# Performance work log

Hardware: AMD Instinct MI355X
Metric: run time of the kernel (lower is better)

Reference implementation:

```python
import jax, jax.numpy as jnp
import numpy as np

N_NODES = 5000
K_POOL = 30
BN_EPS = 1e-5


def setup_inputs() -> dict:
    key = jax.random.key(0)
    ks = jax.random.split(key, 16)
    B, N, Din, C, H, OUT, E = 32, N_NODES, 16, 64, 128, 2, 80000
    F_tot = Din + 3 * C  # concat of input + 3 conv layers = 208
    return {
        "x": jax.random.normal(ks[0], (B, N, Din), jnp.float32),
        "age": jax.random.uniform(ks[1], (B,), jnp.float32) * 100.0,
        "edge_attr": jax.random.uniform(ks[2], (E,), jnp.float32) + 0.1,
        "W0": jax.random.normal(ks[3], (Din, C), jnp.float32) * 0.1,
        "b0": jnp.zeros((C,), jnp.float32),
        "W1": jax.random.normal(ks[4], (C, C), jnp.float32) * 0.1,
        "b1": jnp.zeros((C,), jnp.float32),
        "W2": jax.random.normal(ks[5], (C, C), jnp.float32) * 0.1,
        "b2": jnp.zeros((C,), jnp.float32),
        "g0": jnp.ones((C,), jnp.float32),
        "be0": jnp.zeros((C,), jnp.float32),
        "g1": jnp.ones((C,), jnp.float32),
        "be1": jnp.zeros((C,), jnp.float32),
        "mW0": jax.random.normal(ks[6], (K_POOL * F_tot + 1, H), jnp.float32) * 0.02,
        "mb0": jnp.zeros((H,), jnp.float32),
        "mW1": jax.random.normal(ks[7], (H, OUT), jnp.float32) * 0.1,
        "mb1": jnp.zeros((OUT,), jnp.float32),
        "edge_row": jax.random.randint(ks[8], (E,), 0, N, jnp.int32),
        "edge_col": jax.random.randint(ks[9], (E,), 0, N, jnp.int32),
    }


def _spmm(xw, rows, cols, nv):
    # xw: (B, N, C); out[b, r] = sum_{edges (r,c)} nv * xw[b, c]
    def one(xb):
        return jax.ops.segment_sum(xb[cols] * nv[:, None], rows, num_segments=N_NODES)
    return jax.vmap(one)(xw)


def reference(x, age, edge_attr, W0, b0, W1, b1, W2, b2, g0, be0, g1, be1,
              mW0, mb0, mW1, mb1, edge_row, edge_col):
    N = N_NODES
    # GCN normalization on A + I (gcn_norm with edge weights, self-loop value 1)
    loop = jnp.arange(N, dtype=edge_row.dtype)
    rows = jnp.concatenate([edge_row, loop])
    cols = jnp.concatenate([edge_col, loop])
    vals = jnp.concatenate([edge_attr, jnp.ones((N,), edge_attr.dtype)])
    deg = jax.ops.segment_sum(vals, rows, num_segments=N)
    dinv = jnp.where(deg > 0, jax.lax.rsqrt(jnp.maximum(deg, 1e-12)), 0.0)
    nv = dinv[rows] * vals * dinv[cols]

    feats = [x]
    h = x
    convs = [(W0, b0), (W1, b1), (W2, b2)]
    bns = [(g0, be0), (g1, be1)]
    for i, (W, b) in enumerate(convs):
        h = _spmm(h @ W, rows, cols, nv) + b  # GCNConv
        if i < len(convs) - 1:
            g, be = bns[i]
            mu = jnp.mean(h, axis=(0, 1))   # BatchNorm1d over flattened (B*N, C)
            var = jnp.var(h, axis=(0, 1))
            h = (h - mu) * jax.lax.rsqrt(var + BN_EPS) * g + be
        h = jax.nn.relu(h)  # dropout p=0.0 -> identity
        feats.append(h)

    z = jnp.concatenate(feats, axis=-1)  # (B, N, 208)
    # global_sort_pool: sort nodes by last feature channel, descending, take top-k
    order = jnp.argsort(-z[:, :, -1], axis=1)[:, :K_POOL]  # (B, k)
    zk = jnp.take_along_axis(z, order[:, :, None], axis=1)  # (B, k, 208)
    flat = zk.reshape(z.shape[0], -1)
    flat = jnp.concatenate([flat, age[:, None]], axis=1)  # append age scalar

    hm = jax.nn.relu(flat @ mW0 + mb0)  # MLP head
    out = hm @ mW1 + mb1
    return jax.nn.log_softmax(out, axis=-1)
```

## Files before the change

kernel.cpp:

```cpp
#include <hip/hip_runtime.h>
#include <math.h>

#define NN    5000
#define NE    80000
#define NB    32
#define DIN   16
#define CH    64
#define KPOOL 30
#define FTOT  208
#define FLATW 6241
#define NH    128
#define NG    8
#define GB    4
#define NPB   16
#define NCHUNK 313
#define NPAD  5008
#define NEPAD (NE + 4 * NN)
#define NSLOT 32



__global__ void k_init(float* deg, int* counts, float* stats, float* hm, int* perm) {
    int i = blockIdx.x * 256 + threadIdx.x;
    if (i < NN) { deg[i] = 1.0f; counts[i] = 0; }
    if (i < 2 * NSLOT * 128) stats[i] = 0.0f;
    if (i < 4096) hm[i] = 0.0f;
    if (i >= NN && i < NPAD) perm[i] = NN;
}

#define NEB 313
__global__ void k_edges(const float* __restrict__ attr, const int* __restrict__ erow,
                        float* deg, int* counts) {
    int e = blockIdx.x * 256 + threadIdx.x;
    if (e < NE) {
        int r = erow[e];
        atomicAdd(&deg[r], attr[e]);
        atomicAdd(&counts[r], 1);
    }
}

__global__ __launch_bounds__(1024) void k_phase1(
        const int* __restrict__ counts, const float* __restrict__ deg,
        int* rowptr, int* cursor, float* dinv, int* perm,
        const float* __restrict__ x, float* __restrict__ xt) {
    __shared__ int wsum[16], woff[16];
    __shared__ int carry_sh;
    __shared__ int hist[256];
    int t = threadIdx.x;
    if (blockIdx.x >= 2) {
        int idx = (blockIdx.x - 2) * 1024 + t;
        if (idx >= NB * NN) return;
        int b = idx / NN, n = idx % NN;
        int g = b >> 2, bi = b & 3;
        const float4* src = (const float4*)(x + (size_t)idx * DIN);
        float4* dst = (float4*)(xt + (((size_t)g * NN + n) * GB + bi) * DIN);
        dst[0] = src[0]; dst[1] = src[1]; dst[2] = src[2]; dst[3] = src[3];
        return;
    }
    if (blockIdx.x == 0) {
        int lane = t & 63, wid = t >> 6;
        if (t == 0) carry_sh = 0;
        __syncthreads();
        for (int base = 0; base < NN; base += 1024) {
            int carry = carry_sh;
            int i = base + t;
            int v = 0;
            if (i < NN) {
                v = (counts[i] + 3) & ~3;
                dinv[i] = 1.0f / sqrtf(deg[i]);
            }
            int s = v;
#pragma unroll
            for (int off = 1; off < 64; off <<= 1) {
                int o = __shfl_up(s, off);
                if (lane >= off) s += o;
            }
            if (lane == 63) wsum[wid] = s;
            __syncthreads();
            if (t < 16) {
                int w = wsum[t];
#pragma unroll
                for (int off = 1; off < 16; off <<= 1) {
                    int o = __shfl_up(w, off);
                    if (t >= off) w += o;
                }
                woff[t] = w;
            }
            __syncthreads();
            int inc = s + (wid > 0 ? woff[wid - 1] : 0) + carry;
            if (i < NN) {
                rowptr[i + 1] = inc;
                cursor[i] = inc - v;
            }
            if (t == 1023) carry_sh = carry + woff[15];
            __syncthreads();
        }
        if (t == 0) rowptr[0] = 0;
    } else {
        if (t < 256) hist[t] = 0;
        __syncthreads();
        for (int i = t; i < NN; i += 1024) {
            int b = 255 - min(((counts[i] + 3) & ~3) >> 2, 255);
            atomicAdd(&hist[b], 1);
        }
        __syncthreads();
        int mycnt = (t < 256) ? hist[t] : 0;
        for (int off = 1; off < 256; off <<= 1) {
            int v = (t < 256 && t >= off) ? hist[t - off] : 0;
            __syncthreads();
            if (t < 256) hist[t] += v;
            __syncthreads();
        }
        if (t < 256) hist[t] -= mycnt;
        __syncthreads();
        for (int i = t; i < NN; i += 1024) {
            int b = 255 - min(((counts[i] + 3) & ~3) >> 2, 255);
            int pos = atomicAdd(&hist[b], 1);
            perm[pos] = i;
        }
    }
}

__global__ __launch_bounds__(1024) void k_build(
        const int* __restrict__ erow, const int* __restrict__ ecol,
        const float* __restrict__ attr, const float* __restrict__ dinv,
        const int* __restrict__ counts, const int* __restrict__ rowptr,
        int* cursor, int* csr_col, float* csr_nv) {
    int t = blockIdx.x * 1024 + threadIdx.x;
    if (t < NE) {
        int r = erow[t], c = ecol[t];
        int pos = atomicAdd(&cursor[r], 1);
        csr_col[pos] = c;
        csr_nv[pos] = dinv[r] * attr[t] * dinv[c];
    } else if (t - NE < NN) {
        int i = t - NE;
        int cnt = counts[i];
        int pcnt = (cnt + 3) & ~3;
        int base = rowptr[i + 1] - pcnt;
        for (int p = base + cnt; p < base + pcnt; ++p) { csr_col[p] = i; csr_nv[p] = 0.0f; }
    }
}

template<int ACT>
__device__ __forceinline__ float4 actv(float4 v, float4 s, float4 t) {
    if (ACT) {
        v.x = fmaxf(fmaf(v.x, s.x, t.x), 0.f);
        v.y = fmaxf(fmaf(v.y, s.y, t.y), 0.f);
        v.z = fmaxf(fmaf(v.z, s.z, t.z), 0.f);
        v.w = fmaxf(fmaf(v.w, s.w, t.w), 0.f);
    }
    return v;
}
__device__ __forceinline__ void fma4(float4& a, float w, float4 v) {
    a.x = fmaf(w, v.x, a.x); a.y = fmaf(w, v.y, a.y);
    a.z = fmaf(w, v.z, a.z); a.w = fmaf(w, v.w, a.w);
}

template<int CIN, int ACT, int STATS>
__global__ __launch_bounds__(256) void k_layer(
        const float* __restrict__ in, const float* __restrict__ bnstats,
        const float* __restrict__ gamma, const float* __restrict__ beta,
        const float* __restrict__ W, const float* __restrict__ bias,
        const int* __restrict__ rowptr, const int* __restrict__ csr_col,
        const float* __restrict__ csr_nv, const float* __restrict__ dinv,
        const int* __restrict__ perm,
        float* __restrict__ out, float* __restrict__ stats) {
    constexpr int ALS = (CIN == 64) ? 68 : 20;
    __shared__ float As[4 * 16 * ALS];
    __shared__ float stl[ACT ? 128 : 4];
    int tid = threadIdx.x;
    int wid = tid >> 6, lane = tid & 63;
    int g = blockIdx.x & 7;
    int nb = (blockIdx.x >> 3) * NPB;
    int base = nb + wid * 4;
    float* Aw = As + wid * 16 * ALS;
    const int4 pid = *(const int4*)(perm + base);

    if (ACT) {
        if (tid < 64) {
            float su = 0.f, qu = 0.f;
#pragma unroll
            for (int s = 0; s < NSLOT; ++s) {
                su += bnstats[s * 128 + tid];
                qu += bnstats[s * 128 + 64 + tid];
            }
            const float inv = 1.0f / (float)(NB * NN);
            float mu = su * inv;
            float var = qu * inv - mu * mu;
            float sc = gamma[tid] / sqrtf(var + 1e-5f);
            stl[tid] = sc;
            stl[64 + tid] = fmaf(-mu, sc, beta[tid]);
        }
        __syncthreads();
    }

    if (CIN == 64) {
        const float4* __restrict__ in4 = (const float4*)in + (size_t)g * NN * 64;
        int c4 = lane & 15, bi = lane >> 4;
        float4 sv = {1.f,1.f,1.f,1.f}, tv = {0.f,0.f,0.f,0.f};
        if (ACT) { sv = ((const float4*)stl)[c4]; tv = ((const float4*)(stl + 64))[c4]; }
#pragma unroll
        for (int pr = 0; pr < 2; ++pr) {
            int id0 = (pr == 0) ? pid.x : pid.z;
            int id1 = (pr == 0) ? pid.y : pid.w;
            bool vn0 = id0 < NN, vn1 = id1 < NN;
            int rc0 = vn0 ? id0 : 0, rc1 = vn1 ? id1 : 0;
            float dd0 = dinv[rc0]; dd0 *= dd0;
            float dd1 = dinv[rc1]; dd1 *= dd1;
            float4 a0 = {0.f,0.f,0.f,0.f}, a1 = {0.f,0.f,0.f,0.f};
            {
                float4 v0 = actv<ACT>(in4[(size_t)rc0 * 64 + lane], sv, tv);
                float4 v1 = actv<ACT>(in4[(size_t)rc1 * 64 + lane], sv, tv);
                if (vn0) { a0.x = dd0 * v0.x; a0.y = dd0 * v0.y; a0.z = dd0 * v0.z; a0.w = dd0 * v0.w; }
                if (vn1) { a1.x = dd1 * v1.x; a1.y = dd1 * v1.y; a1.z = dd1 * v1.z; a1.w = dd1 * v1.w; }
            }
            int p0a = rowptr[rc0], na = vn0 ? (rowptr[rc0 + 1] - p0a) >> 2 : 0;
            int p0b = rowptr[rc1], nbv = vn1 ? (rowptr[rc1 + 1] - p0b) >> 2 : 0;
            int mx = max(na, nbv);
            for (int bb = 0; bb < mx; ++bb) {
                int ea = min(p0a + 4 * bb, NEPAD - 4);
                int eb = min(p0b + 4 * bb, NEPAD - 4);
                bool va = bb < na, vb = bb < nbv;
                int4   ca = *(const int4*)(csr_col + ea);
                float4 wa = *(const float4*)(csr_nv + ea);
                int4   cb = *(const int4*)(csr_col + eb);
                float4 wb = *(const float4*)(csr_nv + eb);
                if (!va) { wa.x = 0.f; wa.y = 0.f; wa.z = 0.f; wa.w = 0.f;
                           ca.x = 0; ca.y = 0; ca.z = 0; ca.w = 0; }
                if (!vb) { wb.x = 0.f; wb.y = 0.f; wb.z = 0.f; wb.w = 0.f;
                           cb.x = 0; cb.y = 0; cb.z = 0; cb.w = 0; }
                float4 u0 = in4[(size_t)ca.x * 64 + lane];
                float4 u1 = in4[(size_t)ca.y * 64 + lane];
                float4 u2 = in4[(size_t)ca.z * 64 + lane];
                float4 u3 = in4[(size_t)ca.w * 64 + lane];
                float4 t0 = in4[(size_t)cb.x * 64 + lane];
                float4 t1 = in4[(size_t)cb.y * 64 + lane];
                float4 t2 = in4[(size_t)cb.z * 64 + lane];
                float4 t3 = in4[(size_t)cb.w * 64 + lane];
                fma4(a0, wa.x, actv<ACT>(u0, sv, tv));
                fma4(a0, wa.y, actv<ACT>(u1, sv, tv));
                fma4(a0, wa.z, actv<ACT>(u2, sv, tv));
                fma4(a0, wa.w, actv<ACT>(u3, sv, tv));
                fma4(a1, wb.x, actv<ACT>(t0, sv, tv));
                fma4(a1, wb.y, actv<ACT>(t1, sv, tv));
                fma4(a1, wb.z, actv<ACT>(t2, sv, tv));
                fma4(a1, wb.w, actv<ACT>(t3, sv, tv));
            }
            *(float4*)(Aw + ((pr * 2 + 0) * 4 + bi) * ALS + c4 * 4) = a0;
            *(float4*)(Aw + ((pr * 2 + 1) * 4 + bi) * ALS + c4 * 4) = a1;
        }
    } else {
        const float* __restrict__ inr = in + (size_t)g * NN * 64;
        int ids[4] = {pid.x, pid.y, pid.z, pid.w};
#pragma unroll
        for (int i = 0; i < 4; ++i) {
            int r = ids[i];
            float a = 0.f;
            if (r < NN) {
                float d = dinv[r];
                a = d * d * inr[(size_t)r * 64 + lane];
                int p0 = rowptr[r], p1 = rowptr[r + 1];
                for (int e = p0; e < p1; e += 4) {
                    int4   cc = *(const int4*)(csr_col + e);
                    float4 ww = *(const float4*)(csr_nv + e);
                    float v0 = inr[(size_t)cc.x * 64 + lane];
                    float v1 = inr[(size_t)cc.y * 64 + lane];
                    float v2 = inr[(size_t)cc.z * 64 + lane];
                    float v3 = inr[(size_t)cc.w * 64 + lane];
                    a = fmaf(ww.x, v0, a);
                    a = fmaf(ww.y, v1, a);
                    a = fmaf(ww.z, v2, a);
                    a = fmaf(ww.w, v3, a);
                }
            }
            Aw[(i * 4 + (lane >> 4)) * ALS + (lane & 15)] = a;
        }
    }

    int colq = lane & 15, rowq = lane >> 4;
    int node = (rowq == 0) ? pid.x : (rowq == 1) ? pid.y : (rowq == 2) ? pid.z : pid.w;

    const float4* __restrict__ W4 = (const float4*)W;
    float4 bb = ((const float4*)bias)[colq];
    float4 o[4];
#pragma unroll
    for (int i = 0; i < 4; ++i) o[i] = bb;
#pragma unroll 8
    for (int k = 0; k < CIN; ++k) {
        float4 w4 = W4[k * 16 + colq];
#pragma unroll
        for (int i = 0; i < 4; ++i) {
            float a = Aw[(rowq * 4 + i) * ALS + k];
            fma4(o[i], a, w4);
        }
    }
    if (node < NN) {
        float4* __restrict__ op = (float4*)(out + ((size_t)g * NN + node) * 256);
#pragma unroll
        for (int i = 0; i < 4; ++i) op[i * 16 + colq] = o[i];
    }

    if (STATS) {
        float4 s4 = {0,0,0,0}, q4 = {0,0,0,0};
        if (node < NN) {
#pragma unroll
            for (int i = 0; i < 4; ++i) {
                s4.x += o[i].x; s4.y += o[i].y; s4.z += o[i].z; s4.w += o[i].w;
                q4.x = fmaf(o[i].x, o[i].x, q4.x); q4.y = fmaf(o[i].y, o[i].y, q4.y);
                q4.z = fmaf(o[i].z, o[i].z, q4.z); q4.w = fmaf(o[i].w, o[i].w, q4.w);
            }
        }
        s4.x += __shfl_xor(s4.x, 16); s4.y += __shfl_xor(s4.y, 16);
        s4.z += __shfl_xor(s4.z, 16); s4.w += __shfl_xor(s4.w, 16);
        q4.x += __shfl_xor(q4.x, 16); q4.y += __shfl_xor(q4.y, 16);
        q4.z += __shfl_xor(q4.z, 16); q4.w += __shfl_xor(q4.w, 16);
        s4.x += __shfl_xor(s4.x, 32); s4.y += __shfl_xor(s4.y, 32);
        s4.z += __shfl_xor(s4.z, 32); s4.w += __shfl_xor(s4.w, 32);
        q4.x += __shfl_xor(q4.x, 32); q4.y += __shfl_xor(q4.y, 32);
        q4.z += __shfl_xor(q4.z, 32); q4.w += __shfl_xor(q4.w, 32);
        __syncthreads();
        if (lane < 16) {
            float* S = As + wid * 128;
            *(float4*)(S + lane * 8) = s4;
            *(float4*)(S + lane * 8 + 4) = q4;
        }
        __syncthreads();
        if (tid < 64) {
            int cq = tid >> 2, comp = tid & 3;
            float s = 0.f, q = 0.f;
#pragma unroll
            for (int w = 0; w < 4; ++w) {
                s += As[w * 128 + cq * 8 + comp];
                q += As[w * 128 + cq * 8 + 4 + comp];
            }
            float* sl = stats + (blockIdx.x & (NSLOT - 1)) * 128;
            atomicAdd(&sl[tid], s);
            atomicAdd(&sl[64 + tid], q);
        }
    }
}

#define ZBLK 2048
__global__ __launch_bounds__(256) void k_z(
        const float* __restrict__ h2, const float* __restrict__ bnstats,
        const float* __restrict__ gamma, const float* __restrict__ beta,
        const float* __restrict__ W2, float* __restrict__ z) {
    __shared__ float stl[128];
    __shared__ float w63[64];
    int tid = threadIdx.x;
    if (tid < 64) {
        float su = 0.f, qu = 0.f;
#pragma unroll
        for (int s = 0; s < NSLOT; ++s) {
            su += bnstats[s * 128 + tid];
            qu += bnstats[s * 128 + 64 + tid];
        }
        const float inv = 1.0f / (float)(NB * NN);
        float mu = su * inv;
        float var = qu * inv - mu * mu;
        float sc = gamma[tid] / sqrtf(var + 1e-5f);
        stl[tid] = sc;
        stl[64 + tid] = fmaf(-mu, sc, beta[tid]);
        w63[tid] = W2[tid * 64 + 63];
    }
    __syncthreads();
    int lane = tid & 63, wid = tid >> 6;
    int c4 = lane & 15;
    float4 sv = ((const float4*)stl)[c4];
    float4 tv = ((const float4*)(stl + 64))[c4];
    float4 w4 = ((const float4*)w63)[c4];
    const int total = NB * NN;
    for (int base = blockIdx.x * 16; base < total; base += ZBLK * 16) {
        int row = base + wid * 4 + (lane >> 4);
        float s = 0.f;
        if (row < total) {
            float4 v = ((const float4*)h2)[(size_t)row * 16 + c4];
            v.x = fmaxf(fmaf(v.x, sv.x, tv.x), 0.f);
            v.y = fmaxf(fmaf(v.y, sv.y, tv.y), 0.f);
            v.z = fmaxf(fmaf(v.z, sv.z, tv.z), 0.f);
            v.w = fmaxf(fmaf(v.w, sv.w, tv.w), 0.f);
            s = v.x * w4.x + v.y * w4.y + v.z * w4.z + v.w * w4.w;
        }
        s += __shfl_xor(s, 1);
        s += __shfl_xor(s, 2);
        s += __shfl_xor(s, 4);
        s += __shfl_xor(s, 8);
        if ((lane & 15) == 0 && row < total) z[row] = s;
    }
}

__global__ __launch_bounds__(256) void k_score(
        const float* __restrict__ z, const float* __restrict__ b2,
        const int* __restrict__ rowptr, const int* __restrict__ csr_col,
        const float* __restrict__ csr_nv, const float* __restrict__ dinv,
        float* __restrict__ sc) {
    int tid = threadIdx.x;
    int wid = tid >> 6, lane = tid & 63;
    int g = blockIdx.x & 7;
    int nd = (blockIdx.x >> 3) * 4 + wid;
    if (nd >= NN) return;
    const float4* __restrict__ z4 = (const float4*)z + (size_t)g * NN;
    int p0 = rowptr[nd], p1 = rowptr[nd + 1];
    float4 a = {0.f, 0.f, 0.f, 0.f};
    for (int e = p0 + lane; e < p1; e += 64) {
        int col = csr_col[e];
        float nv = csr_nv[e];
        float4 zv = z4[col];
        fma4(a, nv, zv);
    }
#pragma unroll
    for (int off = 1; off < 64; off <<= 1) {
        a.x += __shfl_xor(a.x, off);
        a.y += __shfl_xor(a.y, off);
        a.z += __shfl_xor(a.z, off);
        a.w += __shfl_xor(a.w, off);
    }
    if (lane == 0) {
        float d = dinv[nd]; d *= d;
        float4 zs = z4[nd];
        float bb = b2[63];
        float4 o;
        o.x = fmaxf(fmaf(d, zs.x, a.x) + bb, 0.f);
        o.y = fmaxf(fmaf(d, zs.y, a.y) + bb, 0.f);
        o.z = fmaxf(fmaf(d, zs.z, a.z) + bb, 0.f);
        o.w = fmaxf(fmaf(d, zs.w, a.w) + bb, 0.f);
        ((float4*)sc)[(size_t)g * NN + nd] = o;
    }
}

__global__ __launch_bounds__(1024) void k_toppool(const float* __restrict__ sc, int* order,
        const float* __restrict__ stats,
        const float* __restrict__ g0, const float* __restrict__ be0,
        const float* __restrict__ g1, const float* __restrict__ be1,
        float* __restrict__ st) {
    __shared__ unsigned long long wbest[16];
    __shared__ unsigned long long winner;
    int tid = threadIdx.x;
    if (blockIdx.x == NB) {
        if (tid < 128) {
            int c = tid & 63, layer = tid >> 6;
            const float* sb = stats + layer * NSLOT * 128;
            float su = 0.f, qu = 0.f;
#pragma unroll
            for (int s = 0; s < NSLOT; ++s) {
                su += sb[s * 128 + c];
                qu += sb[s * 128 + 64 + c];
            }
            const float inv = 1.0f / (float)(NB * NN);
            float mu = su * inv;
            float var = qu * inv - mu * mu;
            float g = layer ? g1[c] : g0[c];
            float be = layer ? be1[c] : be0[c];
            float scv = g / sqrtf(var + 1e-5f);
            st[layer * 128 + c] = scv;
            st[layer * 128 + 64 + c] = fmaf(-mu, scv, be);
        }
        return;
    }
    int b = blockIdx.x;
    int g = b >> 2, bi = b & 3;
    int lane = tid & 63, wid = tid >> 6;
    unsigned long long key[5];
#pragma unroll
    for (int j = 0; j < 5; ++j) {
        int n = tid + j * 1024;
        unsigned long long k = 0;
        if (n < NN) {
            float v = sc[((size_t)g * NN + n) * GB + bi];
            k = ((unsigned long long)__float_as_uint(v) << 32) | (unsigned int)(NN - n);
        }
        key[j] = k;
    }
    for (int k = 0; k < KPOOL; ++k) {
        unsigned long long best = key[0];
#pragma unroll
        for (int j = 1; j < 5; ++j) best = (key[j] > best) ? key[j] : best;
#pragma unroll
        for (int off = 1; off < 64; off <<= 1) {
            unsigned long long o = __shfl_xor(best, off);
            best = (o > best) ? o : best;
        }
        if (lane == 0) wbest[wid] = best;
        __syncthreads();
        if (tid == 0) {
            unsigned long long w = wbest[0];
#pragma unroll
            for (int i = 1; i < 16; ++i) w = (wbest[i] > w) ? wbest[i] : w;
            winner = w;
            order[b * KPOOL + k] = NN - (int)(w & 0xFFFFFFFFu);
        }
        __syncthreads();
        int n = NN - (int)(winner & 0xFFFFFFFFu);
        if ((n & 1023) == tid) key[n >> 10] = 0;
    }
}

__global__ void k_gather(const float* __restrict__ xt, const float* __restrict__ h1,
                         const float* __restrict__ h2,
                         const float* __restrict__ W2, const float* __restrict__ b2,
                         const float* __restrict__ st, const float* __restrict__ age,
                         const int* __restrict__ rowptr, const int* __restrict__ csr_col,
                         const float* __restrict__ csr_nv, const float* __restrict__ dinv,
                         const int* __restrict__ order, float* __restrict__ flat) {
    __shared__ float aggP[4][64];
    __shared__ float aggRow[64];
    int bk = blockIdx.x;
    int b = bk / KPOOL, k = bk % KPOOL;
    int n = order[bk];
    int g = b >> 2, bi = b & 3;
    size_t node = (size_t)g * NN + n;
    int tid = threadIdx.x;
    {
        int ep = tid >> 6, c = tid & 63;
        float sc1 = st[128 + c], sh1 = st[192 + c];
        float a = 0.f;
        if (ep == 0) {
            float d = dinv[n];
            float v = h2[(node * GB + bi) * CH + c];
            a = d * d * fmaxf(fmaf(v, sc1, sh1), 0.f);
        }
        int p0 = rowptr[n], p1 = rowptr[n + 1];
        for (int e = p0 + ep; e < p1; e += 4) {
            int col = csr_col[e];
            float nv = csr_nv[e];
            float v = h2[(((size_t)g * NN + col) * GB + bi) * CH + c];
            a += nv * fmaxf(fmaf(v, sc1, sh1), 0.f);
        }
        aggP[ep][c] = a;
    }
    __syncthreads();
    if (tid < 64) aggRow[tid] = aggP[0][tid] + aggP[1][tid] + aggP[2][tid] + aggP[3][tid];
    __syncthreads();
    int f = tid;
    float val = 0.f;
    if (f < DIN) {
        val = xt[(node * GB + bi) * DIN + f];
    } else if (f < DIN + CH) {
        int c = f - DIN;
        val = fmaxf(fmaf(h1[(node * GB + bi) * CH + c], st[c], st[64 + c]), 0.f);
    } else if (f < DIN + 2 * CH) {
        int c = f - DIN - CH;
        val = fmaxf(fmaf(h2[(node * GB + bi) * CH + c], st[128 + c], st[192 + c]), 0.f);
    } else if (f < FTOT) {
        int c = f - DIN - 2 * CH;
        float s = b2[c];
#pragma unroll 8
        for (int kk = 0; kk < 64; ++kk)
            s = fmaf(aggRow[kk], W2[kk * 64 + c], s);
        val = fmaxf(s, 0.f);
    }
    if (f < FTOT) flat[(size_t)b * FLATW + k * FTOT + f] = val;
    if (bk == 0 && f >= FTOT && f < FTOT + NB)
        flat[(size_t)(f - FTOT) * FLATW + (FLATW - 1)] = age[f - FTOT];
}

__global__ void k_head1(const float* __restrict__ flat, const float* __restrict__ mW0,
                        float* hm) {
    int tid = threadIdx.x;
    int j4 = (tid & 31) * 4;
    int b0 = (tid >> 5) * 4;
    int kbase = blockIdx.x * 64;
    float acc[4][4];
#pragma unroll
    for (int i = 0; i < 4; i++)
#pragma unroll
        for (int jj = 0; jj < 4; jj++) acc[i][jj] = 0.f;
    int kend = FLATW - kbase; if (kend > 64) kend = 64;
    for (int kk = 0; kk < kend; ++kk) {
        int k = kbase + kk;
        float4 w = *(const float4*)(mW0 + (size_t)k * NH + j4);
#pragma unroll
        for (int i = 0; i < 4; i++) {
            float fv = flat[(size_t)(b0 + i) * FLATW + k];
            acc[i][0] = fmaf(fv, w.x, acc[i][0]);
            acc[i][1] = fmaf(fv, w.y, acc[i][1]);
            acc[i][2] = fmaf(fv, w.z, acc[i][2]);
            acc[i][3] = fmaf(fv, w.w, acc[i][3]);
        }
    }
#pragma unroll
    for (int i = 0; i < 4; i++)
#pragma unroll
        for (int jj = 0; jj < 4; jj++)
            atomicAdd(&hm[(size_t)(b0 + i) * NH + j4 + jj], acc[i][jj]);
}

__global__ void k_head2(const float* __restrict__ hm, const float* __restrict__ mb0,
                        const float* __restrict__ mW1, const float* __restrict__ mb1,
                        float* __restrict__ out) {
    __shared__ float part[256];
    __shared__ float vals[64];
    int tid = threadIdx.x;
    int q = tid & 3, o = (tid >> 2) & 1, b = tid >> 3;
    float acc = 0.f;
    for (int j = q * 32; j < q * 32 + 32; ++j) {
        float hv = fmaxf(hm[b * NH + j] + mb0[j], 0.f);
        acc = fmaf(hv, mW1[j * 2 + o], acc);
    }
    part[tid] = acc;
    __syncthreads();
    if (tid < 64) {
        int b2 = tid >> 1, o2 = tid & 1;
        int base = (b2 << 3) + (o2 << 2);
        vals[tid] = part[base] + part[base + 1] + part[base + 2] + part[base + 3] + mb1[o2];
    }
    __syncthreads();
    if (tid < 64) {
        int b2 = tid >> 1;
        float v0 = vals[b2 * 2], v1 = vals[b2 * 2 + 1];
        float m = fmaxf(v0, v1);
        float lse = m + logf(expf(v0 - m) + expf(v1 - m));
        out[tid] = vals[tid] - lse;
    }
}

extern "C" void kernel_launch(void* const* d_in, const int* in_sizes, int n_in,
                              void* d_out, int out_size, void* d_ws, size_t ws_size,
                              hipStream_t stream) {
    const float* x    = (const float*)d_in[0];
    const float* age  = (const float*)d_in[1];
    const float* attr = (const float*)d_in[2];
    const float* W0   = (const float*)d_in[3];
    const float* b0   = (const float*)d_in[4];
    const float* W1   = (const float*)d_in[5];
    const float* b1   = (const float*)d_in[6];
    const float* W2   = (const float*)d_in[7];
    const float* b2   = (const float*)d_in[8];
    const float* g0   = (const float*)d_in[9];
    const float* be0  = (const float*)d_in[10];
    const float* g1   = (const float*)d_in[11];
    const float* be1  = (const float*)d_in[12];
    const float* mW0  = (const float*)d_in[13];
    const float* mb0  = (const float*)d_in[14];
    const float* mW1  = (const float*)d_in[15];
    const float* mb1  = (const float*)d_in[16];
    const int* erow   = (const int*)d_in[17];
    const int* ecol   = (const int*)d_in[18];
    float* out = (float*)d_out;

    float* ws     = (float*)d_ws;
    float* deg    = ws;
    float* dinv   = deg + 5008;
    int*   counts = (int*)(dinv + 5008);
    int*   rowptr = counts + 5008;
    int*   cursor = rowptr + 5008;
    int*   perm   = cursor + 5008;
    int*   csr_col= perm + 5008;
    float* csr_nv = (float*)(csr_col + NEPAD);
    float* stats  = csr_nv + NEPAD;
    float* st     = stats + 2 * NSLOT * 128;
    float* sc     = st + 256;
    int*   order  = (int*)(sc + NB * NN);
    float* flat   = (float*)(order + 960);
    float* hm     = flat + (size_t)NB * FLATW;
    float* xt     = hm + 4096;
    float* h1     = xt + (size_t)NB * NN * DIN;
    float* h2     = h1 + (size_t)NB * NN * CH;
    float* z      = h2 + (size_t)NB * NN * CH;

    k_init<<<32, 256, 0, stream>>>(deg, counts, stats, hm, perm);
    k_edges<<<NEB, 256, 0, stream>>>(attr, erow, deg, counts);
    k_phase1<<<2 + (NB * NN + 1023) / 1024, 1024, 0, stream>>>(counts, deg, rowptr, cursor, dinv, perm, x, xt);
    k_build<<<(NE + NN + 1023) / 1024, 1024, 0, stream>>>(erow, ecol, attr, dinv, counts, rowptr, cursor, csr_col, csr_nv);

    const int NBLK = NCHUNK * NG;
    k_layer<16, 0, 1><<<NBLK, 256, 0, stream>>>(xt, nullptr, nullptr, nullptr, W0, b0, rowptr, csr_col, csr_nv, dinv, perm, h1, stats);
    k_layer<64, 1, 1><<<NBLK, 256, 0, stream>>>(h1, stats, g0, be0, W1, b1, rowptr, csr_col, csr_nv, dinv, perm, h2, stats + NSLOT * 128);
    k_z<<<ZBLK, 256, 0, stream>>>(h2, stats + NSLOT * 128, g1, be1, W2, z);
    k_score<<<(NN / 4) * NG, 256, 0, stream>>>(z, b2, rowptr, csr_col, csr_nv, dinv, sc);

    k_toppool<<<NB + 1, 1024, 0, stream>>>(sc, order, stats, g0, be0, g1, be1, st);
    k_gather<<<NB * KPOOL, 256, 0, stream>>>(xt, h1, h2, W2, b2, st, age, rowptr, csr_col, csr_nv, dinv, order, flat);
    k_head1<<<(FLATW + 63) / 64, 256, 0, stream>>>(flat, mW0, hm);
    k_head2<<<1, 256, 0, stream>>>(hm, mb0, mW1, mb1, out);
}
```

Measured before the change: 316.5 us.

## Regroup input into 8-batch groups and specialize first GCN layer with float2 gathers

Changes the transposed input layout from 4-batch to 8-batch groups so each 64-lane wavefront gathers a full neighbor row (8 batches x 16 channels) as float2 per lane. It adds a dedicated first-layer kernel that processes 8 batches per block with half as many blocks. The old template splits into separate 16- and 64-channel kernels. The aim is better-utilized, wider gathers and fewer redundant CSR index loads in layer 0. In exchange it uses more registers for 8 output accumulators, and the gather kernel's read of the input must follow the new layout.

```diff
diff --git a/kernel.cpp b/kernel.cpp
--- a/kernel.cpp
+++ b/kernel.cpp
@@ -51,9 +51,9 @@
         int idx = (blockIdx.x - 2) * 1024 + t;
         if (idx >= NB * NN) return;
         int b = idx / NN, n = idx % NN;
-        int g = b >> 2, bi = b & 3;
+        int g4 = b >> 3, bi8 = b & 7;
         const float4* src = (const float4*)(x + (size_t)idx * DIN);
-        float4* dst = (float4*)(xt + (((size_t)g * NN + n) * GB + bi) * DIN);
+        float4* dst = (float4*)(xt + (((size_t)g4 * NN + n) * 8 + bi8) * DIN);
         dst[0] = src[0]; dst[1] = src[1]; dst[2] = src[2]; dst[3] = src[3];
         return;
     }
@@ -141,23 +141,154 @@
     }
 }
 
-template<int ACT>
 __device__ __forceinline__ float4 actv(float4 v, float4 s, float4 t) {
-    if (ACT) {
-        v.x = fmaxf(fmaf(v.x, s.x, t.x), 0.f);
-        v.y = fmaxf(fmaf(v.y, s.y, t.y), 0.f);
-        v.z = fmaxf(fmaf(v.z, s.z, t.z), 0.f);
-        v.w = fmaxf(fmaf(v.w, s.w, t.w), 0.f);
-    }
+    v.x = fmaxf(fmaf(v.x, s.x, t.x), 0.f);
+    v.y = fmaxf(fmaf(v.y, s.y, t.y), 0.f);
+    v.z = fmaxf(fmaf(v.z, s.z, t.z), 0.f);
+    v.w = fmaxf(fmaf(v.w, s.w, t.w), 0.f);
     return v;
 }
 __device__ __forceinline__ void fma4(float4& a, float w, float4 v) {
     a.x = fmaf(w, v.x, a.x); a.y = fmaf(w, v.y, a.y);
     a.z = fmaf(w, v.z, a.z); a.w = fmaf(w, v.w, a.w);
 }
-
-template<int CIN, int ACT, int STATS>
-__global__ __launch_bounds__(256) void k_layer(
+__device__ __forceinline__ void fma2(float2& a, float w, float2 v) {
+    a.x = fmaf(w, v.x, a.x); a.y = fmaf(w, v.y, a.y);
+}
+
+__global__ __launch_bounds__(256) void k_l16(
+        const float* __restrict__ in,
+        const float* __restrict__ W, const float* __restrict__ bias,
+        const int* __restrict__ rowptr, const int* __restrict__ csr_col,
+        const float* __restrict__ csr_nv, const float* __restrict__ dinv,
+        const int* __restrict__ perm,
+        float* __restrict__ out, float* __restrict__ stats) {
+    const int ALS = 18;
+    __shared__ float As[4 * 32 * ALS];
+    int tid = threadIdx.x;
+    int wid = tid >> 6, lane = tid & 63;
+    int g4 = blockIdx.x & 3;
+    int base = (blockIdx.x >> 2) * NPB + wid * 4;
+    float* Aw = As + wid * 32 * ALS;
+    const int4 pid = *(const int4*)(perm + base);
+
+    const float2* __restrict__ in2 = (const float2*)in + (size_t)g4 * NN * 64;
+    int bi8 = lane >> 3, chp = lane & 7;
+
+#pragma unroll
+    for (int pr = 0; pr < 2; ++pr) {
+        int id0 = (pr == 0) ? pid.x : pid.z;
+        int id1 = (pr == 0) ? pid.y : pid.w;
+        bool vn0 = id0 < NN, vn1 = id1 < NN;
+        int rc0 = vn0 ? id0 : 0, rc1 = vn1 ? id1 : 0;
+        float dd0 = dinv[rc0]; dd0 *= dd0;
+        float dd1 = dinv[rc1]; dd1 *= dd1;
+        float2 a0 = {0.f, 0.f}, a1 = {0.f, 0.f};
+        {
+            float2 v0 = in2[(size_t)rc0 * 64 + lane];
+            float2 v1 = in2[(size_t)rc1 * 64 + lane];
+            if (vn0) { a0.x = dd0 * v0.x; a0.y = dd0 * v0.y; }
+            if (vn1) { a1.x = dd1 * v1.x; a1.y = dd1 * v1.y; }
+        }
+        int p0a = rowptr[rc0], na = vn0 ? (rowptr[rc0 + 1] - p0a) >> 2 : 0;
+        int p0b = rowptr[rc1], nbv = vn1 ? (rowptr[rc1 + 1] - p0b) >> 2 : 0;
+        int mx = max(na, nbv);
+        for (int bb = 0; bb < mx; ++bb) {
+            int ea = min(p0a + 4 * bb, NEPAD - 4);
+            int eb = min(p0b + 4 * bb, NEPAD - 4);
+            bool va = bb < na, vb = bb < nbv;
+            int4   ca = *(const int4*)(csr_col + ea);
+            float4 wa = *(const float4*)(csr_nv + ea);
+            int4   cb = *(const int4*)(csr_col + eb);
+            float4 wb = *(const float4*)(csr_nv + eb);
+            if (!va) { wa.x = 0.f; wa.y = 0.f; wa.z = 0.f; wa.w = 0.f;
+                       ca.x = 0; ca.y = 0; ca.z = 0; ca.w = 0; }
+            if (!vb) { wb.x = 0.f; wb.y = 0.f; wb.z = 0.f; wb.w = 0.f;
+                       cb.x = 0; cb.y = 0; cb.z = 0; cb.w = 0; }
+            float2 u0 = in2[(size_t)ca.x * 64 + lane];
+            float2 u1 = in2[(size_t)ca.y * 64 + lane];
+            float2 u2 = in2[(size_t)ca.z * 64 + lane];
+            float2 u3 = in2[(size_t)ca.w * 64 + lane];
+            float2 t0 = in2[(size_t)cb.x * 64 + lane];
+            float2 t1 = in2[(size_t)cb.y * 64 + lane];
+            float2 t2 = in2[(size_t)cb.z * 64 + lane];
+            float2 t3 = in2[(size_t)cb.w * 64 + lane];
+            fma2(a0, wa.x, u0);
+            fma2(a0, wa.y, u1);
+            fma2(a0, wa.z, u2);
+            fma2(a0, wa.w, u3);
+            fma2(a1, wb.x, t0);
+            fma2(a1, wb.y, t1);
+            fma2(a1, wb.z, t2);
+            fma2(a1, wb.w, t3);
+        }
+        *(float2*)(Aw + ((2 * pr + 0) * 8 + bi8) * ALS + chp * 2) = a0;
+        *(float2*)(Aw + ((2 * pr + 1) * 8 + bi8) * ALS + chp * 2) = a1;
+    }
+
+    int colq = lane & 15, rowq = lane >> 4;
+    int node = (rowq == 0) ? pid.x : (rowq == 1) ? pid.y : (rowq == 2) ? pid.z : pid.w;
+
+    const float4* __restrict__ W4 = (const float4*)W;
+    float4 bb4 = ((const float4*)bias)[colq];
+    float4 o[8];
+#pragma unroll
+    for (int i = 0; i < 8; ++i) o[i] = bb4;
+#pragma unroll
+    for (int k = 0; k < 16; ++k) {
+        float4 w4 = W4[k * 16 + colq];
+#pragma unroll
+        for (int i = 0; i < 8; ++i)
+            fma4(o[i], Aw[(rowq * 8 + i) * ALS + k], w4);
+    }
+    if (node < NN) {
+#pragma unroll
+        for (int i = 0; i < 8; ++i) {
+            int g8 = g4 * 2 + (i >> 2);
+            float4* op = (float4*)(out + (((size_t)g8 * NN + node) * 4 + (i & 3)) * 64);
+            op[colq] = o[i];
+        }
+    }
+
+    float4 s4 = {0,0,0,0}, q4 = {0,0,0,0};
+    if (node < NN) {
+#pragma unroll
+        for (int i = 0; i < 8; ++i) {
+            s4.x += o[i].x; s4.y += o[i].y; s4.z += o[i].z; s4.w += o[i].w;
+            q4.x = fmaf(o[i].x, o[i].x, q4.x); q4.y = fmaf(o[i].y, o[i].y, q4.y);
+            q4.z = fmaf(o[i].z, o[i].z, q4.z); q4.w = fmaf(o[i].w, o[i].w, q4.w);
+        }
+    }
+    s4.x += __shfl_xor(s4.x, 16); s4.y += __shfl_xor(s4.y, 16);
+    s4.z += __shfl_xor(s4.z, 16); s4.w += __shfl_xor(s4.w, 16);
+    q4.x += __shfl_xor(q4.x, 16); q4.y += __shfl_xor(q4.y, 16);
+    q4.z += __shfl_xor(q4.z, 16); q4.w += __shfl_xor(q4.w, 16);
+    s4.x += __shfl_xor(s4.x, 32); s4.y += __shfl_xor(s4.y, 32);
+    s4.z += __shfl_xor(s4.z, 32); s4.w += __shfl_xor(s4.w, 32);
+    q4.x += __shfl_xor(q4.x, 32); q4.y += __shfl_xor(q4.y, 32);
+    q4.z += __shfl_xor(q4.z, 32); q4.w += __shfl_xor(q4.w, 32);
+    __syncthreads();
+    if (lane < 16) {
+        float* S = As + wid * 128;
+        *(float4*)(S + lane * 8) = s4;
+        *(float4*)(S + lane * 8 + 4) = q4;
+    }
+    __syncthreads();
+    if (tid < 64) {
+        int cq = tid >> 2, comp = tid & 3;
+        float s = 0.f, q = 0.f;
+#pragma unroll
+        for (int w = 0; w < 4; ++w) {
+            s += As[w * 128 + cq * 8 + comp];
+            q += As[w * 128 + cq * 8 + 4 + comp];
+        }
+        float* sl = stats + (blockIdx.x & (NSLOT - 1)) * 128;
+        atomicAdd(&sl[tid], s);
+        atomicAdd(&sl[64 + tid], q);
+    }
+}
+
+__global__ __launch_bounds__(256) void k_l64(
         const float* __restrict__ in, const float* __restrict__ bnstats,
         const float* __restrict__ gamma, const float* __restrict__ beta,
         const float* __restrict__ W, const float* __restrict__ bias,
@@ -165,116 +296,85 @@
         const float* __restrict__ csr_nv, const float* __restrict__ dinv,
         const int* __restrict__ perm,
         float* __restrict__ out, float* __restrict__ stats) {
-    constexpr int ALS = (CIN == 64) ? 68 : 20;
+    const int ALS = 68;
     __shared__ float As[4 * 16 * ALS];
-    __shared__ float stl[ACT ? 128 : 4];
+    __shared__ float stl[128];
     int tid = threadIdx.x;
     int wid = tid >> 6, lane = tid & 63;
     int g = blockIdx.x & 7;
-    int nb = (blockIdx.x >> 3) * NPB;
-    int base = nb + wid * 4;
+    int base = (blockIdx.x >> 3) * NPB + wid * 4;
     float* Aw = As + wid * 16 * ALS;
     const int4 pid = *(const int4*)(perm + base);
 
-    if (ACT) {
-        if (tid < 64) {
-            float su = 0.f, qu = 0.f;
-#pragma unroll
-            for (int s = 0; s < NSLOT; ++s) {
-                su += bnstats[s * 128 + tid];
-                qu += bnstats[s * 128 + 64 + tid];
-            }
-            const float inv = 1.0f / (float)(NB * NN);
-            float mu = su * inv;
-            float var = qu * inv - mu * mu;
-            float sc = gamma[tid] / sqrtf(var + 1e-5f);
-            stl[tid] = sc;
-            stl[64 + tid] = fmaf(-mu, sc, beta[tid]);
-        }
-        __syncthreads();
-    }
-
-    if (CIN == 64) {
-        const float4* __restrict__ in4 = (const float4*)in + (size_t)g * NN * 64;
-        int c4 = lane & 15, bi = lane >> 4;
-        float4 sv = {1.f,1.f,1.f,1.f}, tv = {0.f,0.f,0.f,0.f};
-        if (ACT) { sv = ((const float4*)stl)[c4]; tv = ((const float4*)(stl + 64))[c4]; }
-#pragma unroll
-        for (int pr = 0; pr < 2; ++pr) {
-            int id0 = (pr == 0) ? pid.x : pid.z;
-            int id1 = (pr == 0) ? pid.y : pid.w;
-            bool vn0 = id0 < NN, vn1 = id1 < NN;
-            int rc0 = vn0 ? id0 : 0, rc1 = vn1 ? id1 : 0;
-            float dd0 = dinv[rc0]; dd0 *= dd0;
-            float dd1 = dinv[rc1]; dd1 *= dd1;
-            float4 a0 = {0.f,0.f,0.f,0.f}, a1 = {0.f,0.f,0.f,0.f};
-            {
-                float4 v0 = actv<ACT>(in4[(size_t)rc0 * 64 + lane], sv, tv);
-                float4 v1 = actv<ACT>(in4[(size_t)rc1 * 64 + lane], sv, tv);
-                if (vn0) { a0.x = dd0 * v0.x; a0.y = dd0 * v0.y; a0.z = dd0 * v0.z; a0.w = dd0 * v0.w; }
-                if (vn1) { a1.x = dd1 * v1.x; a1.y = dd1 * v1.y; a1.z = dd1 * v1.z; a1.w = dd1 * v1.w; }
-            }
-            int p0a = rowptr[rc0], na = vn0 ? (rowptr[rc0 + 1] - p0a) >> 2 : 0;
-            int p0b = rowptr[rc1], nbv = vn1 ? (rowptr[rc1 + 1] - p0b) >> 2 : 0;
-            int mx = max(na, nbv);
-            for (int bb = 0; bb < mx; ++bb) {
-                int ea = min(p0a + 4 * bb, NEPAD - 4);
-                int eb = min(p0b + 4 * bb, NEPAD - 4);
-                bool va = bb < na, vb = bb < nbv;
-                int4   ca = *(const int4*)(csr_col + ea);
-                float4 wa = *(const float4*)(csr_nv + ea);
-                int4   cb = *(const int4*)(csr_col + eb);
-                float4 wb = *(const float4*)(csr_nv + eb);
-                if (!va) { wa.x = 0.f; wa.y = 0.f; wa.z = 0.f; wa.w = 0.f;
-                           ca.x = 0; ca.y = 0; ca.z = 0; ca.w = 0; }
-                if (!vb) { wb.x = 0.f; wb.y = 0.f; wb.z = 0.f; wb.w = 0.f;
-                           cb.x = 0; cb.y = 0; cb.z = 0; cb.w = 0; }
-                float4 u0 = in4[(size_t)ca.x * 64 + lane];
-                float4 u1 = in4[(size_t)ca.y * 64 + lane];
-                float4 u2 = in4[(size_t)ca.z * 64 + lane];
-                float4 u3 = in4[(size_t)ca.w * 64 + lane];
-                float4 t0 = in4[(size_t)cb.x * 64 + lane];
-                float4 t1 = in4[(size_t)cb.y * 64 + lane];
-                float4 t2 = in4[(size_t)cb.z * 64 + lane];
-                float4 t3 = in4[(size_t)cb.w * 64 + lane];
-                fma4(a0, wa.x, actv<ACT>(u0, sv, tv));
-                fma4(a0, wa.y, actv<ACT>(u1, sv, tv));
-                fma4(a0, wa.z, actv<ACT>(u2, sv, tv));
-                fma4(a0, wa.w, actv<ACT>(u3, sv, tv));
-                fma4(a1, wb.x, actv<ACT>(t0, sv, tv));
-                fma4(a1, wb.y, actv<ACT>(t1, sv, tv));
-                fma4(a1, wb.z, actv<ACT>(t2, sv, tv));
-                fma4(a1, wb.w, actv<ACT>(t3, sv, tv));
-            }
-            *(float4*)(Aw + ((pr * 2 + 0) * 4 + bi) * ALS + c4 * 4) = a0;
-            *(float4*)(Aw + ((pr * 2 + 1) * 4 + bi) * ALS + c4 * 4) = a1;
-        }
-    } else {
-        const float* __restrict__ inr = in + (size_t)g * NN * 64;
-        int ids[4] = {pid.x, pid.y, pid.z, pid.w};
-#pragma unroll
-        for (int i = 0; i < 4; ++i) {
-            int r = ids[i];
-            float a = 0.f;
-            if (r < NN) {
-                float d = dinv[r];
-                a = d * d * inr[(size_t)r * 64 + lane];
-                int p0 = rowptr[r], p1 = rowptr[r + 1];
-                for (int e = p0; e < p1; e += 4) {
-                    int4   cc = *(const int4*)(csr_col + e);
-                    float4 ww = *(const float4*)(csr_nv + e);
-                    float v0 = inr[(size_t)cc.x * 64 + lane];
-                    float v1 = inr[(size_t)cc.y * 64 + lane];
-                    float v2 = inr[(size_t)cc.z * 64 + lane];
-                    float v3 = inr[(size_t)cc.w * 64 + lane];
-                    a = fmaf(ww.x, v0, a);
-                    a = fmaf(ww.y, v1, a);
-                    a = fmaf(ww.z, v2, a);
-                    a = fmaf(ww.w, v3, a);
-                }
-            }
-            Aw[(i * 4 + (lane >> 4)) * ALS + (lane & 15)] = a;
-        }
+    if (tid < 64) {
+        float su = 0.f, qu = 0.f;
+#pragma unroll
+        for (int s = 0; s < NSLOT; ++s) {
+            su += bnstats[s * 128 + tid];
+            qu += bnstats[s * 128 + 64 + tid];
+        }
+        const float inv = 1.0f / (float)(NB * NN);
+        float mu = su * inv;
+        float var = qu * inv - mu * mu;
+        float sc = gamma[tid] / sqrtf(var + 1e-5f);
+        stl[tid] = sc;
+        stl[64 + tid] = fmaf(-mu, sc, beta[tid]);
+    }
+    __syncthreads();
+
+    const float4* __restrict__ in4 = (const float4*)in + (size_t)g * NN * 64;
+    int c4 = lane & 15, bi = lane >> 4;
+    float4 sv = ((const float4*)stl)[c4];
+    float4 tv = ((const float4*)(stl + 64))[c4];
+#pragma unroll
+    for (int pr = 0; pr < 2; ++pr) {
+        int id0 = (pr == 0) ? pid.x : pid.z;
+        int id1 = (pr == 0) ? pid.y : pid.w;
+        bool vn0 = id0 < NN, vn1 = id1 < NN;
+        int rc0 = vn0 ? id0 : 0, rc1 = vn1 ? id1 : 0;
+        float dd0 = dinv[rc0]; dd0 *= dd0;
+        float dd1 = dinv[rc1]; dd1 *= dd1;
+        float4 a0 = {0.f,0.f,0.f,0.f}, a1 = {0.f,0.f,0.f,0.f};
+        {
+            float4 v0 = actv(in4[(size_t)rc0 * 64 + lane], sv, tv);
+            float4 v1 = actv(in4[(size_t)rc1 * 64 + lane], sv, tv);
+            if (vn0) { a0.x = dd0 * v0.x; a0.y = dd0 * v0.y; a0.z = dd0 * v0.z; a0.w = dd0 * v0.w; }
+            if (vn1) { a1.x = dd1 * v1.x; a1.y = dd1 * v1.y; a1.z = dd1 * v1.z; a1.w = dd1 * v1.w; }
+        }
+        int p0a = rowptr[rc0], na = vn0 ? (rowptr[rc0 + 1] - p0a) >> 2 : 0;
+        int p0b = rowptr[rc1], nbv = vn1 ? (rowptr[rc1 + 1] - p0b) >> 2 : 0;
+        int mx = max(na, nbv);
+        for (int bb = 0; bb < mx; ++bb) {
+            int ea = min(p0a + 4 * bb, NEPAD - 4);
+            int eb = min(p0b + 4 * bb, NEPAD - 4);
+            bool va = bb < na, vb = bb < nbv;
+            int4   ca = *(const int4*)(csr_col + ea);
+            float4 wa = *(const float4*)(csr_nv + ea);
+            int4   cb = *(const int4*)(csr_col + eb);
+            float4 wb = *(const float4*)(csr_nv + eb);
+            if (!va) { wa.x = 0.f; wa.y = 0.f; wa.z = 0.f; wa.w = 0.f;
+                       ca.x = 0; ca.y = 0; ca.z = 0; ca.w = 0; }
+            if (!vb) { wb.x = 0.f; wb.y = 0.f; wb.z = 0.f; wb.w = 0.f;
+                       cb.x = 0; cb.y = 0; cb.z = 0; cb.w = 0; }
+            float4 u0 = in4[(size_t)ca.x * 64 + lane];
+            float4 u1 = in4[(size_t)ca.y * 64 + lane];
+            float4 u2 = in4[(size_t)ca.z * 64 + lane];
+            float4 u3 = in4[(size_t)ca.w * 64 + lane];
+            float4 t0 = in4[(size_t)cb.x * 64 + lane];
+            float4 t1 = in4[(size_t)cb.y * 64 + lane];
+            float4 t2 = in4[(size_t)cb.z * 64 + lane];
+            float4 t3 = in4[(size_t)cb.w * 64 + lane];
+            fma4(a0, wa.x, actv(u0, sv, tv));
+            fma4(a0, wa.y, actv(u1, sv, tv));
+            fma4(a0, wa.z, actv(u2, sv, tv));
+            fma4(a0, wa.w, actv(u3, sv, tv));
+            fma4(a1, wb.x, actv(t0, sv, tv));
+            fma4(a1, wb.y, actv(t1, sv, tv));
+            fma4(a1, wb.z, actv(t2, sv, tv));
+            fma4(a1, wb.w, actv(t3, sv, tv));
+        }
+        *(float4*)(Aw + ((pr * 2 + 0) * 4 + bi) * ALS + c4 * 4) = a0;
+        *(float4*)(Aw + ((pr * 2 + 1) * 4 + bi) * ALS + c4 * 4) = a1;
     }
 
     int colq = lane & 15, rowq = lane >> 4;
@@ -286,7 +386,7 @@
 #pragma unroll
     for (int i = 0; i < 4; ++i) o[i] = bb;
 #pragma unroll 8
-    for (int k = 0; k < CIN; ++k) {
+    for (int k = 0; k < 64; ++k) {
         float4 w4 = W4[k * 16 + colq];
 #pragma unroll
         for (int i = 0; i < 4; ++i) {
@@ -300,43 +400,41 @@
         for (int i = 0; i < 4; ++i) op[i * 16 + colq] = o[i];
     }
 
-    if (STATS) {
-        float4 s4 = {0,0,0,0}, q4 = {0,0,0,0};
-        if (node < NN) {
-#pragma unroll
-            for (int i = 0; i < 4; ++i) {
-                s4.x += o[i].x; s4.y += o[i].y; s4.z += o[i].z; s4.w += o[i].w;
-                q4.x = fmaf(o[i].x, o[i].x, q4.x); q4.y = fmaf(o[i].y, o[i].y, q4.y);
-                q4.z = fmaf(o[i].z, o[i].z, q4.z); q4.w = fmaf(o[i].w, o[i].w, q4.w);
-            }
-        }
-        s4.x += __shfl_xor(s4.x, 16); s4.y += __shfl_xor(s4.y, 16);
-        s4.z += __shfl_xor(s4.z, 16); s4.w += __shfl_xor(s4.w, 16);
-        q4.x += __shfl_xor(q4.x, 16); q4.y += __shfl_xor(q4.y, 16);
-        q4.z += __shfl_xor(q4.z, 16); q4.w += __shfl_xor(q4.w, 16);
-        s4.x += __shfl_xor(s4.x, 32); s4.y += __shfl_xor(s4.y, 32);
-        s4.z += __shfl_xor(s4.z, 32); s4.w += __shfl_xor(s4.w, 32);
-        q4.x += __shfl_xor(q4.x, 32); q4.y += __shfl_xor(q4.y, 32);
-        q4.z += __shfl_xor(q4.z, 32); q4.w += __shfl_xor(q4.w, 32);
-        __syncthreads();
-        if (lane < 16) {
-            float* S = As + wid * 128;
-            *(float4*)(S + lane * 8) = s4;
-            *(float4*)(S + lane * 8 + 4) = q4;
-        }
-        __syncthreads();
-        if (tid < 64) {
-            int cq = tid >> 2, comp = tid & 3;
-            float s = 0.f, q = 0.f;
-#pragma unroll
-            for (int w = 0; w < 4; ++w) {
-                s += As[w * 128 + cq * 8 + comp];
-                q += As[w * 128 + cq * 8 + 4 + comp];
-            }
-            float* sl = stats + (blockIdx.x & (NSLOT - 1)) * 128;
-            atomicAdd(&sl[tid], s);
-            atomicAdd(&sl[64 + tid], q);
-        }
+    float4 s4 = {0,0,0,0}, q4 = {0,0,0,0};
+    if (node < NN) {
+#pragma unroll
+        for (int i = 0; i < 4; ++i) {
+            s4.x += o[i].x; s4.y += o[i].y; s4.z += o[i].z; s4.w += o[i].w;
+            q4.x = fmaf(o[i].x, o[i].x, q4.x); q4.y = fmaf(o[i].y, o[i].y, q4.y);
+            q4.z = fmaf(o[i].z, o[i].z, q4.z); q4.w = fmaf(o[i].w, o[i].w, q4.w);
+        }
+    }
+    s4.x += __shfl_xor(s4.x, 16); s4.y += __shfl_xor(s4.y, 16);
+    s4.z += __shfl_xor(s4.z, 16); s4.w += __shfl_xor(s4.w, 16);
+    q4.x += __shfl_xor(q4.x, 16); q4.y += __shfl_xor(q4.y, 16);
+    q4.z += __shfl_xor(q4.z, 16); q4.w += __shfl_xor(q4.w, 16);
+    s4.x += __shfl_xor(s4.x, 32); s4.y += __shfl_xor(s4.y, 32);
+    s4.z += __shfl_xor(s4.z, 32); s4.w += __shfl_xor(s4.w, 32);
+    q4.x += __shfl_xor(q4.x, 32); q4.y += __shfl_xor(q4.y, 32);
+    q4.z += __shfl_xor(q4.z, 32); q4.w += __shfl_xor(q4.w, 32);
+    __syncthreads();
+    if (lane < 16) {
+        float* S = As + wid * 128;
+        *(float4*)(S + lane * 8) = s4;
+        *(float4*)(S + lane * 8 + 4) = q4;
+    }
+    __syncthreads();
+    if (tid < 64) {
+        int cq = tid >> 2, comp = tid & 3;
+        float s = 0.f, q = 0.f;
+#pragma unroll
+        for (int w = 0; w < 4; ++w) {
+            s += As[w * 128 + cq * 8 + comp];
+            q += As[w * 128 + cq * 8 + 4 + comp];
+        }
+        float* sl = stats + (blockIdx.x & (NSLOT - 1)) * 128;
+        atomicAdd(&sl[tid], s);
+        atomicAdd(&sl[64 + tid], q);
     }
 }
 
@@ -534,7 +632,7 @@
     int f = tid;
     float val = 0.f;
     if (f < DIN) {
-        val = xt[(node * GB + bi) * DIN + f];
+        val = xt[(((size_t)(b >> 3) * NN + n) * 8 + (b & 7)) * DIN + f];
     } else if (f < DIN + CH) {
         int c = f - DIN;
         val = fmaxf(fmaf(h1[(node * GB + bi) * CH + c], st[c], st[64 + c]), 0.f);
@@ -663,9 +761,8 @@
     k_phase1<<<2 + (NB * NN + 1023) / 1024, 1024, 0, stream>>>(counts, deg, rowptr, cursor, dinv, perm, x, xt);
     k_build<<<(NE + NN + 1023) / 1024, 1024, 0, stream>>>(erow, ecol, attr, dinv, counts, rowptr, cursor, csr_col, csr_nv);
 
-    const int NBLK = NCHUNK * NG;
-    k_layer<16, 0, 1><<<NBLK, 256, 0, stream>>>(xt, nullptr, nullptr, nullptr, W0, b0, rowptr, csr_col, csr_nv, dinv, perm, h1, stats);
-    k_layer<64, 1, 1><<<NBLK, 256, 0, stream>>>(h1, stats, g0, be0, W1, b1, rowptr, csr_col, csr_nv, dinv, perm, h2, stats + NSLOT * 128);
+    k_l16<<<NCHUNK * 4, 256, 0, stream>>>(xt, W0, b0, rowptr, csr_col, csr_nv, dinv, perm, h1, stats);
+    k_l64<<<NCHUNK * NG, 256, 0, stream>>>(h1, stats, g0, be0, W1, b1, rowptr, csr_col, csr_nv, dinv, perm, h2, stats + NSLOT * 128);
     k_z<<<ZBLK, 256, 0, stream>>>(h2, stats + NSLOT * 128, g1, be1, W2, z);
     k_score<<<(NN / 4) * NG, 256, 0, stream>>>(z, b2, rowptr, csr_col, csr_nv, dinv, sc);
 
```

Result: no change. 318.4 us (+0.6%).
